# Kernel optimization log

Measured on AMD Instinct MI355X. Metric: run time of the kernel, lower is better.

The kernel has to match this reference:

```python
import jax, jax.numpy as jnp
import numpy as np

B, S, T = 1024, 1024, 32  # batch, seq_len, num_tags


def setup_inputs() -> dict:
    key = jax.random.key(0)
    k1, k2, k3, k4 = jax.random.split(key, 4)
    logits = jax.random.normal(k1, (B, S, T), dtype=jnp.float32)
    transitions = jax.random.normal(k2, (T, T), dtype=jnp.float32)
    tags = jax.random.randint(k3, (B, S), 0, T)
    lengths = jax.random.randint(k4, (B,), 1, S + 1)
    return {"logits": logits, "transitions": transitions, "tags": tags, "lengths": lengths}


def _forward_alg(logits, transitions):
    # viterbi_0 = logits[:, 0, :]; then for t>=1:
    # v_next[b, j] = logsumexp_i(v[b, i] + trans[i, j]) + logits[b, t, j]
    v0 = logits[:, 0, :]  # (B, T)
    emits = jnp.swapaxes(logits[:, 1:, :], 0, 1)  # (S-1, B, T)

    def step(v, emit_t):
        v_next = jax.nn.logsumexp(v[:, :, None] + transitions[None, :, :], axis=1) + emit_t
        return v_next, None

    v_final, _ = jax.lax.scan(step, v0, emits)
    return jax.nn.logsumexp(v_final, axis=1)  # (B,)


def _score_sentence(logits, transitions, tags, lengths):
    # emission scores of gold tags, masked to t < length (note: original ignores
    # lengths in the forward algorithm but uses them here, faithfully reproduced)
    emit = jnp.take_along_axis(logits, tags[:, :, None], axis=2)[..., 0]  # (B, S)
    pos = jnp.arange(S)
    emit_mask = (pos[None, :] < lengths[:, None]).astype(logits.dtype)
    score = jnp.sum(emit * emit_mask, axis=1)
    # transition scores trans[tags[t-1], tags[t]] for 1 <= t < length
    trans_sc = transitions[tags[:, :-1], tags[:, 1:]]  # (B, S-1)
    trans_mask = (pos[None, 1:] < lengths[:, None]).astype(logits.dtype)
    score = score + jnp.sum(trans_sc * trans_mask, axis=1)
    return score  # (B,)


def reference(logits, transitions, tags, lengths):
    log_z = _forward_alg(logits, transitions)
    gold = _score_sentence(logits, transitions, tags, lengths)
    return jnp.mean(log_z - gold)
```

## Files before the change

kernel.cpp:

```cpp
#include <hip/hip_runtime.h>

#define NB 1024
#define NS 1024
#define NT 32
#define L2E 1.44269504088896340736f
#define LN2 0.69314718055994530942f

typedef short        bfrag  __attribute__((ext_vector_type(8)));
typedef float        cfrag  __attribute__((ext_vector_type(16)));
typedef __bf16       bf16x2 __attribute__((ext_vector_type(2)));
typedef float        f32x8  __attribute__((ext_vector_type(8)));
typedef float        f32x4  __attribute__((ext_vector_type(4)));
typedef float        f32x2  __attribute__((ext_vector_type(2)));
typedef unsigned int u32;
typedef unsigned int u32x4  __attribute__((ext_vector_type(4)));

__device__ __forceinline__ float fexp2(float x){ return __builtin_amdgcn_exp2f(x); }
__device__ __forceinline__ float flog2(float x){ return __builtin_amdgcn_logf(x); }

__device__ __forceinline__ u32 pkbf_rne(float a, float b){
    f32x2 t; t.x = a; t.y = b;
    return __builtin_bit_cast(u32, __builtin_convertvector(t, bf16x2));
}
__device__ __forceinline__ u32 pkbf_t(float a, float b){
    return __builtin_amdgcn_perm(__builtin_bit_cast(u32, b),
                                 __builtin_bit_cast(u32, a), 0x07060302u);
}
__device__ __forceinline__ bfrag mk_afrag(f32x8 v){
    u32x4 r;
    r[0] = pkbf_rne(v[0], v[1]); r[1] = pkbf_rne(v[2], v[3]);
    r[2] = pkbf_rne(v[4], v[5]); r[3] = pkbf_rne(v[6], v[7]);
    return __builtin_bit_cast(bfrag, r);
}

__device__ __forceinline__ int rho(int k){
    int bb = (k >> 2) & 3;
    return (bb == 1 || bb == 2) ? (k ^ 12) : k;
}

template<int N> struct ic { static constexpr int value = N; };
union accu { cfrag c; f32x2 p[8]; };
union q4u  { f32x4 v; f32x2 p[2]; };

__global__ __launch_bounds__(256, 8) void crf_chunk(
    const float* __restrict__ logits, const float* __restrict__ trans,
    const int* __restrict__ tags, const int* __restrict__ lens,
    u32* __restrict__ wmat, float* __restrict__ woff, float* __restrict__ gpart)
{
    __shared__ __align__(16) float dscall[4 * 512];

    const int tid = threadIdx.x;
    const int wv  = tid >> 6, lt = tid & 63;
    const int m   = lt & 31,  h  = lt >> 5;
    const int bc  = blockIdx.x * 4 + wv;
    const int b   = bc >> 3,  c  = bc & 7;
    float* dsc = dscall + wv * 512;

    const float* base = logits + (size_t)b * NS * NT;
    const int    len  = lens[b];
    const int    tb   = b * NS;

    f32x8 Et0, Et1;
    #pragma unroll
    for (int j = 0; j < 8; j++){
        Et0[j] = fexp2(L2E * trans[rho(     8*h + j)*NT + m]);
        Et1[j] = fexp2(L2E * trans[rho(16 + 8*h + j)*NT + m]);
    }
    const bfrag A0f = mk_afrag(Et0);
    const bfrag A1f = mk_afrag(Et1);

    u32x4 B0v, B1v;
    #pragma unroll
    for (int d = 0; d < 4; d++){
        int k0 = 8*h + 2*d;      u32 v = 0;
        if (rho(k0)     == m) v |= 0x3F80u;
        if (rho(k0 + 1) == m) v |= 0x3F800000u;
        B0v[d] = v;
        int k1 = 16 + 8*h + 2*d; v = 0;
        if (rho(k1)     == m) v |= 0x3F80u;
        if (rho(k1 + 1) == m) v |= 0x3F800000u;
        B1v[d] = v;
    }

    cfrag zacc;
    #pragma unroll
    for (int q = 0; q < 16; q++) zacc[q] = 0.0f;

    int   offi = 0;
    float exf  = 0.0f;
    float g    = 0.0f;
    const int tbeg = c*128 + 1;

    float eA[4], eB[4];

    auto issue = [&](float (&e)[4], int k){
        const int t0 = tbeg + k*8 + 4*h;
        #pragma unroll
        for (int i = 0; i < 4; i++){
            int t = t0 + i; t = t > (NS-1) ? (NS-1) : t;
            e[i] = base[t*NT + m];
        }
    };
    auto commit = [&](float (&e)[4], int k){
        float* sp = dsc + (k & 1)*256 + (4*h)*32 + m;
        float a0 = (h == 0) ? -exf : 0.0f;
        sp[0]    = fexp2(fmaf(L2E, e[0], a0));
        sp[32]   = fexp2(L2E * e[1]);
        sp[64]   = fexp2(L2E * e[2]);
        sp[96]   = fexp2(L2E * e[3]);
        const int t0 = tbeg + k*8 + 4*h;
        int tp = tags[tb + t0 - 1];
        #pragma unroll
        for (int i = 0; i < 4; i++){
            int t  = t0 + i;
            int tc = tags[tb + (t > (NS-1) ? (NS-1) : t)];
            float contrib = e[i] + trans[tp*NT + tc];
            if (t < len && m == tc) g += contrib;
            tp = tc;
        }
    };

    auto exref = [&](float ref)->int{
        u32 xb = __builtin_bit_cast(u32, ref);
        u32 xf = __builtin_amdgcn_readfirstlane(xb);
        int ex = (int)((xf >> 23) & 0xFFu) - 127;
        return ex < -120 ? -120 : (ex > 120 ? 120 : ex);
    };

    auto procN = [&](int k, bool defer, auto nstc){
        constexpr int NST = decltype(nstc)::value;
        const float* db = dsc + (k & 1)*256 + 4*h;
        #pragma unroll
        for (int i = 0; i < NST; i++){
            accu acc;
            acc.c = __builtin_amdgcn_mfma_f32_32x32x16_bf16(
                        A0f, __builtin_bit_cast(bfrag, B0v), zacc, 0, 0, 0);
            acc.c = __builtin_amdgcn_mfma_f32_32x32x16_bf16(
                        A1f, __builtin_bit_cast(bfrag, B1v), acc.c, 0, 0, 0);

            q4u d0, d1, d2, d3;
            d0.v = *(const f32x4*)(db + i*32 +  0);
            d1.v = *(const f32x4*)(db + i*32 +  8);
            d2.v = *(const f32x4*)(db + i*32 + 16);
            d3.v = *(const f32x4*)(db + i*32 + 24);
            acc.p[0] *= d0.p[0]; acc.p[1] *= d0.p[1];
            acc.p[2] *= d1.p[0]; acc.p[3] *= d1.p[1];
            acc.p[4] *= d2.p[0]; acc.p[5] *= d2.p[1];
            acc.p[6] *= d3.p[0]; acc.p[7] *= d3.p[1];

            if (i == 3){
                int ex = exref(fmaxf(acc.c[0], acc.c[8]));
                offi += ex;
                f32x2 s2;
                s2.x = s2.y = __builtin_bit_cast(float, (u32)(127 - ex) << 23);
                #pragma unroll
                for (int q = 0; q < 8; q++) acc.p[q] *= s2;
            }
            if (i == 7 && defer){
                int ex = exref(fmaxf(acc.c[0], acc.c[8]));
                offi += ex;
                exf = (float)ex;
            }

            B0v[0] = pkbf_t(acc.c[0],  acc.c[1]);  B0v[1] = pkbf_t(acc.c[2],  acc.c[3]);
            B0v[2] = pkbf_t(acc.c[4],  acc.c[5]);  B0v[3] = pkbf_t(acc.c[6],  acc.c[7]);
            B1v[0] = pkbf_t(acc.c[8],  acc.c[9]);  B1v[1] = pkbf_t(acc.c[10], acc.c[11]);
            B1v[2] = pkbf_t(acc.c[12], acc.c[13]); B1v[3] = pkbf_t(acc.c[14], acc.c[15]);
        }
    };

    issue(eA, 0); commit(eA, 0);
    #pragma unroll 1
    for (int k = 0; k < 14; k += 2){
        issue(eB, k + 1);
        procN(k, true, ic<8>{});
        commit(eB, k + 1);
        issue(eA, k + 2);
        procN(k + 1, true, ic<8>{});
        commit(eA, k + 2);
    }
    issue(eB, 15);
    procN(14, true, ic<8>{});
    commit(eB, 15);
    if (c != 7) procN(15, false, ic<8>{});
    else        procN(15, false, ic<7>{});

    const size_t mb = (size_t)bc * 512;
    #pragma unroll
    for (int d = 0; d < 4; d++){
        wmat[mb + d*64 + lt]     = B0v[d];
        wmat[mb + (4+d)*64 + lt] = B1v[d];
    }
    if (lt == 0) woff[bc] = (float)offi;

    #pragma unroll
    for (int d = 1; d < 64; d <<= 1) g += __shfl_xor(g, d, 64);
    if (lt == 0) gpart[bc] = g;
}

__global__ __launch_bounds__(64) void crf_combine(
    const float* __restrict__ logits, const int* __restrict__ tags,
    const u32* __restrict__ wmat, const float* __restrict__ woff,
    const float* __restrict__ gpart, float* __restrict__ out)
{
    __shared__ __align__(16) float ldsU[NT];

    const int tid = threadIdx.x;
    const int m   = tid & 31;
    const int b   = blockIdx.x;
    const float* lgb = logits + (size_t)b * NS * NT;

    const int   tg0 = tags[(size_t)b * NS];
    const float e0  = lgb[tg0];

    float4 gp0 = ((const float4*)(gpart + b*8))[0];
    float4 gp1 = ((const float4*)(gpart + b*8))[1];
    const float gsum = (gp0.x + gp0.y) + (gp0.z + gp0.w)
                     + (gp1.x + gp1.y) + (gp1.z + gp1.w);

    float offs[8];
    #pragma unroll
    for (int cc = 0; cc < 8; cc++) offs[cc] = woff[b*8 + cc];

    float v    = fexp2(L2E * lgb[m]);
    float voff = 0.0f;

    const int n  = m;
    const int bb = (n >> 2) & 3;
    const int nn = (bb == 1 || bb == 2) ? (n ^ 12) : n;
    const int f  = nn >> 4;
    const int hh = (nn >> 3) & 1;
    const int di = f*4 + ((nn >> 1) & 3);
    const int lo = nn & 1;

    auto ldrow = [&](int cc, uint4 (&md)[8]){
        const uint4* mp = (const uint4*)(wmat + (size_t)(b*8 + cc)*512 + di*64 + hh*32);
        #pragma unroll
        for (int qq = 0; qq < 8; qq++) md[qq] = mp[qq];
    };

    uint4 mdA[8], mdB[8];
    ldrow(0, mdA);

    #pragma unroll
    for (int cc = 0; cc < 8; cc++){
        uint4 (&cur)[8] = (cc & 1) ? mdB : mdA;
        uint4 (&nxt)[8] = (cc & 1) ? mdA : mdB;
        if (cc < 7) ldrow(cc + 1, nxt);

        float w  = flog2(v) + offs[cc];
        float mw = w;
        #pragma unroll
        for (int d = 1; d <= 16; d <<= 1) mw = fmaxf(mw, __shfl_xor(mw, d, 64));
        float u = fexp2(w - mw);
        if (tid < 32) ldsU[m] = u;
        __syncthreads();

        float acc = 0.0f;
        #pragma unroll
        for (int qq = 0; qq < 8; qq++){
            uint4  md = cur[qq];
            float4 uu = ((const float4*)ldsU)[qq];
            float v0 = __builtin_bit_cast(float, lo ? (md.x & 0xFFFF0000u) : (md.x << 16));
            float v1 = __builtin_bit_cast(float, lo ? (md.y & 0xFFFF0000u) : (md.y << 16));
            float v2 = __builtin_bit_cast(float, lo ? (md.z & 0xFFFF0000u) : (md.z << 16));
            float v3 = __builtin_bit_cast(float, lo ? (md.w & 0xFFFF0000u) : (md.w << 16));
            acc = fmaf(v0, uu.x, acc);
            acc = fmaf(v1, uu.y, acc);
            acc = fmaf(v2, uu.z, acc);
            acc = fmaf(v3, uu.w, acc);
        }
        v = acc;
        voff += mw;
        __syncthreads();
    }

    float s = v;
    #pragma unroll
    for (int d = 1; d <= 16; d <<= 1) s += __shfl_xor(s, d, 64);
    if (tid == 0){
        float logz = LN2 * (voff + flog2(s));
        atomicAdd(out, (logz - gsum - e0) * (1.0f / (float)NB));
    }
}

extern "C" void kernel_launch(void* const* d_in, const int* in_sizes, int n_in,
                              void* d_out, int out_size, void* d_ws, size_t ws_size,
                              hipStream_t stream) {
    const float* logits = (const float*)d_in[0];
    const float* trans  = (const float*)d_in[1];
    const int*   tags   = (const int*)d_in[2];
    const int*   lens   = (const int*)d_in[3];

    u32*   wmat  = (u32*)d_ws;
    float* woff  = (float*)(wmat + 8192*512);
    float* gpart = woff + 8192;

    hipMemsetAsync(d_out, 0, sizeof(float), stream);
    crf_chunk  <<<2048, 256, 0, stream>>>(logits, trans, tags, lens, wmat, woff, gpart);
    crf_combine<<<1024,  64, 0, stream>>>(logits, tags, wmat, woff, gpart, (float*)d_out);
}
```

Before: 309.0 us.

## Move gold-path scoring from chunk kernel into combine kernel and drop memset

The gold-score gather (tags, transitions, emissions) is removed from the latency-critical chunk kernel's commit loop and recomputed in the combine kernel, which now runs 256 threads per batch and stages tags and transitions in LDS. The output zeroing moves from a separate memset into the first thread of the chunk kernel, removing one launch. This shortens the serial recurrence critical path at the cost of extra gathered loads in the combine kernel. The zeroing relies on the chunk kernel finishing before the combine kernel's atomics, which stream ordering provides.

```diff
diff --git a/kernel.cpp b/kernel.cpp
--- a/kernel.cpp
+++ b/kernel.cpp
@@ -44,8 +44,7 @@
 
 __global__ __launch_bounds__(256, 8) void crf_chunk(
     const float* __restrict__ logits, const float* __restrict__ trans,
-    const int* __restrict__ tags, const int* __restrict__ lens,
-    u32* __restrict__ wmat, float* __restrict__ woff, float* __restrict__ gpart)
+    u32* __restrict__ wmat, float* __restrict__ woff, float* __restrict__ outz)
 {
     __shared__ __align__(16) float dscall[4 * 512];
 
@@ -56,9 +55,9 @@
     const int b   = bc >> 3,  c  = bc & 7;
     float* dsc = dscall + wv * 512;
 
+    if (blockIdx.x == 0 && tid == 0) *outz = 0.0f;
+
     const float* base = logits + (size_t)b * NS * NT;
-    const int    len  = lens[b];
-    const int    tb   = b * NS;
 
     f32x8 Et0, Et1;
     #pragma unroll
@@ -88,7 +87,6 @@
 
     int   offi = 0;
     float exf  = 0.0f;
-    float g    = 0.0f;
     const int tbeg = c*128 + 1;
 
     float eA[4], eB[4];
@@ -108,16 +106,6 @@
         sp[32]   = fexp2(L2E * e[1]);
         sp[64]   = fexp2(L2E * e[2]);
         sp[96]   = fexp2(L2E * e[3]);
-        const int t0 = tbeg + k*8 + 4*h;
-        int tp = tags[tb + t0 - 1];
-        #pragma unroll
-        for (int i = 0; i < 4; i++){
-            int t  = t0 + i;
-            int tc = tags[tb + (t > (NS-1) ? (NS-1) : t)];
-            float contrib = e[i] + trans[tp*NT + tc];
-            if (t < len && m == tc) g += contrib;
-            tp = tc;
-        }
     };
 
     auto exref = [&](float ref)->int{
@@ -192,31 +180,49 @@
         wmat[mb + (4+d)*64 + lt] = B1v[d];
     }
     if (lt == 0) woff[bc] = (float)offi;
-
-    #pragma unroll
-    for (int d = 1; d < 64; d <<= 1) g += __shfl_xor(g, d, 64);
-    if (lt == 0) gpart[bc] = g;
-}
-
-__global__ __launch_bounds__(64) void crf_combine(
-    const float* __restrict__ logits, const int* __restrict__ tags,
+}
+
+__global__ __launch_bounds__(256) void crf_combine(
+    const float* __restrict__ logits, const float* __restrict__ trans,
+    const int* __restrict__ tags, const int* __restrict__ lens,
     const u32* __restrict__ wmat, const float* __restrict__ woff,
-    const float* __restrict__ gpart, float* __restrict__ out)
+    float* __restrict__ out)
 {
+    __shared__ __align__(16) float ldsT[NT*NT];
+    __shared__ __align__(16) int   ldsTag[NS];
     __shared__ __align__(16) float ldsU[NT];
+    __shared__ float red[4];
 
     const int tid = threadIdx.x;
     const int m   = tid & 31;
     const int b   = blockIdx.x;
+    const int len = lens[b];
     const float* lgb = logits + (size_t)b * NS * NT;
 
-    const int   tg0 = tags[(size_t)b * NS];
-    const float e0  = lgb[tg0];
-
-    float4 gp0 = ((const float4*)(gpart + b*8))[0];
-    float4 gp1 = ((const float4*)(gpart + b*8))[1];
-    const float gsum = (gp0.x + gp0.y) + (gp0.z + gp0.w)
-                     + (gp1.x + gp1.y) + (gp1.z + gp1.w);
+    ((float4*)ldsT)[tid] = ((const float4*)trans)[tid];
+    ((int4*)ldsTag)[tid] = ((const int4*)(tags + (size_t)b * NS))[tid];
+    __syncthreads();
+
+    const int t0 = tid * 4;
+    int4 tgv = ((const int4*)ldsTag)[tid];
+    int  prv = ldsTag[tid == 0 ? 0 : t0 - 1];
+    int tgs[5] = {prv, tgv.x, tgv.y, tgv.z, tgv.w};
+
+    float g = 0.0f;
+    #pragma unroll
+    for (int i = 0; i < 4; i++){
+        int t = t0 + i;
+        if (t < len){
+            float e  = lgb[t*NT + tgs[i+1]];
+            float tr = (t >= 1) ? ldsT[tgs[i]*NT + tgs[i+1]] : 0.0f;
+            g += e + tr;
+        }
+    }
+    #pragma unroll
+    for (int d = 1; d < 64; d <<= 1) g += __shfl_xor(g, d, 64);
+    if ((tid & 63) == 0) red[tid >> 6] = g;
+    __syncthreads();
+    const float gsum = red[0] + red[1] + red[2] + red[3];
 
     float offs[8];
     #pragma unroll
@@ -280,7 +286,7 @@
     for (int d = 1; d <= 16; d <<= 1) s += __shfl_xor(s, d, 64);
     if (tid == 0){
         float logz = LN2 * (voff + flog2(s));
-        atomicAdd(out, (logz - gsum - e0) * (1.0f / (float)NB));
+        atomicAdd(out, (logz - gsum) * (1.0f / (float)NB));
     }
 }
 
@@ -292,11 +298,10 @@
     const int*   tags   = (const int*)d_in[2];
     const int*   lens   = (const int*)d_in[3];
 
-    u32*   wmat  = (u32*)d_ws;
-    float* woff  = (float*)(wmat + 8192*512);
-    float* gpart = woff + 8192;
-
-    hipMemsetAsync(d_out, 0, sizeof(float), stream);
-    crf_chunk  <<<2048, 256, 0, stream>>>(logits, trans, tags, lens, wmat, woff, gpart);
-    crf_combine<<<1024,  64, 0, stream>>>(logits, tags, wmat, woff, gpart, (float*)d_out);
-}
+    u32*   wmat = (u32*)d_ws;
+    float* woff = (float*)(wmat + 8192*512);
+
+    crf_chunk  <<<2048, 256, 0, stream>>>(logits, trans, wmat, woff, (float*)d_out);
+    crf_combine<<<1024, 256, 0, stream>>>(logits, trans, tags, lens, wmat, woff,
+                                          (float*)d_out);
+}
```

New measurement: 261.7 us. 15.3% less time.

## Fuse chunk and combine kernels via last-block-done atomic counter

Applied to the files above, without the earlier changes.

Merges the per-chunk forward kernel and the per-batch combine kernel into one launch. The last wave to finish a batch row, detected through an atomic counter, runs the 8-step matrix combine. The combine now broadcasts the vector with wave shuffles instead of LDS and barriers, and rescales by a power-of-two exponent instead of log/exp. The gold-path score is moved out of the inner commit loop into a single vectorized pass per wave that accumulates atomically. This removes a kernel launch and the intermediate gpart round trip, at the cost of extra atomics and threadfences and a serialized tail on the last-arriving waves.

```diff
diff --git a/kernel.cpp b/kernel.cpp
--- a/kernel.cpp
+++ b/kernel.cpp
@@ -32,6 +32,9 @@
     r[2] = pkbf_rne(v[4], v[5]); r[3] = pkbf_rne(v[6], v[7]);
     return __builtin_bit_cast(bfrag, r);
 }
+__device__ __forceinline__ float ubf(u32 x, int lo){
+    return __builtin_bit_cast(float, lo ? (x & 0xFFFF0000u) : (x << 16));
+}
 
 __device__ __forceinline__ int rho(int k){
     int bb = (k >> 2) & 3;
@@ -42,10 +45,13 @@
 union accu { cfrag c; f32x2 p[8]; };
 union q4u  { f32x4 v; f32x2 p[2]; };
 
-__global__ __launch_bounds__(256, 8) void crf_chunk(
+__global__ __launch_bounds__(256, 8) void crf_fused(
     const float* __restrict__ logits, const float* __restrict__ trans,
     const int* __restrict__ tags, const int* __restrict__ lens,
-    u32* __restrict__ wmat, float* __restrict__ woff, float* __restrict__ gpart)
+    u32* __restrict__ wmat, float* __restrict__ woff,
+    float* __restrict__ gacc, int* __restrict__ cnt,
+    float* __restrict__ outac, int* __restrict__ nfin,
+    float* __restrict__ out)
 {
     __shared__ __align__(16) float dscall[4 * 512];
 
@@ -88,7 +94,6 @@
 
     int   offi = 0;
     float exf  = 0.0f;
-    float g    = 0.0f;
     const int tbeg = c*128 + 1;
 
     float eA[4], eB[4];
@@ -108,16 +113,6 @@
         sp[32]   = fexp2(L2E * e[1]);
         sp[64]   = fexp2(L2E * e[2]);
         sp[96]   = fexp2(L2E * e[3]);
-        const int t0 = tbeg + k*8 + 4*h;
-        int tp = tags[tb + t0 - 1];
-        #pragma unroll
-        for (int i = 0; i < 4; i++){
-            int t  = t0 + i;
-            int tc = tags[tb + (t > (NS-1) ? (NS-1) : t)];
-            float contrib = e[i] + trans[tp*NT + tc];
-            if (t < len && m == tc) g += contrib;
-            tp = tc;
-        }
     };
 
     auto exref = [&](float ref)->int{
@@ -193,94 +188,87 @@
     }
     if (lt == 0) woff[bc] = (float)offi;
 
-    #pragma unroll
-    for (int d = 1; d < 64; d <<= 1) g += __shfl_xor(g, d, 64);
-    if (lt == 0) gpart[bc] = g;
-}
-
-__global__ __launch_bounds__(64) void crf_combine(
-    const float* __restrict__ logits, const int* __restrict__ tags,
-    const u32* __restrict__ wmat, const float* __restrict__ woff,
-    const float* __restrict__ gpart, float* __restrict__ out)
-{
-    __shared__ __align__(16) float ldsU[NT];
-
-    const int tid = threadIdx.x;
-    const int m   = tid & 31;
-    const int b   = blockIdx.x;
-    const float* lgb = logits + (size_t)b * NS * NT;
-
-    const int   tg0 = tags[(size_t)b * NS];
-    const float e0  = lgb[tg0];
-
-    float4 gp0 = ((const float4*)(gpart + b*8))[0];
-    float4 gp1 = ((const float4*)(gpart + b*8))[1];
-    const float gsum = (gp0.x + gp0.y) + (gp0.z + gp0.w)
-                     + (gp1.x + gp1.y) + (gp1.z + gp1.w);
+    {
+        const int t1 = tbeg + 2*lt;
+        const int t2 = t1 + 1;
+        const int i2 = t2 > (NS-1) ? (NS-1) : t2;
+        const int g0 = tags[tb + t1 - 1];
+        const int g1 = tags[tb + t1];
+        const int g2 = tags[tb + i2];
+        float gg = 0.0f;
+        if (t1 < len) gg += base[t1*NT + g1] + trans[g0*NT + g1];
+        if (t2 < len) gg += base[t2*NT + g2] + trans[g1*NT + g2];
+        #pragma unroll
+        for (int d = 1; d < 64; d <<= 1) gg += __shfl_xor(gg, d, 64);
+        if (lt == 0){
+            if (c == 0) gg += base[tags[tb]];
+            atomicAdd(&gacc[b], gg);
+        }
+    }
+
+    __threadfence();
+    int old = 0;
+    if (lt == 0) old = atomicAdd(&cnt[b], 1);
+    old = __shfl(old, 0, 64);
+    if (old != 7) return;
+
+    __threadfence();
+
+    const int n   = lt & 31;
+    const int bb2 = (n >> 2) & 3;
+    const int nn  = (bb2 == 1 || bb2 == 2) ? (n ^ 12) : n;
+    const int segbase = (nn >> 4)*256 + ((nn >> 3) & 1)*32 + ((nn >> 1) & 3)*64;
+    const int lo  = nn & 1;
+    const u32* wbm = wmat + (size_t)b * 8 * 512 + segbase;
 
     float offs[8];
     #pragma unroll
     for (int cc = 0; cc < 8; cc++) offs[cc] = woff[b*8 + cc];
 
-    float v    = fexp2(L2E * lgb[m]);
+    float v    = fexp2(L2E * base[n]);
     float voff = 0.0f;
 
-    const int n  = m;
-    const int bb = (n >> 2) & 3;
-    const int nn = (bb == 1 || bb == 2) ? (n ^ 12) : n;
-    const int f  = nn >> 4;
-    const int hh = (nn >> 3) & 1;
-    const int di = f*4 + ((nn >> 1) & 3);
-    const int lo = nn & 1;
-
-    auto ldrow = [&](int cc, uint4 (&md)[8]){
-        const uint4* mp = (const uint4*)(wmat + (size_t)(b*8 + cc)*512 + di*64 + hh*32);
+    #pragma unroll
+    for (int cc = 0; cc < 8; cc++){
+        uint4 md[8];
+        const uint4* mp = (const uint4*)(wbm + cc*512);
         #pragma unroll
         for (int qq = 0; qq < 8; qq++) md[qq] = mp[qq];
-    };
-
-    uint4 mdA[8], mdB[8];
-    ldrow(0, mdA);
-
-    #pragma unroll
-    for (int cc = 0; cc < 8; cc++){
-        uint4 (&cur)[8] = (cc & 1) ? mdB : mdA;
-        uint4 (&nxt)[8] = (cc & 1) ? mdA : mdB;
-        if (cc < 7) ldrow(cc + 1, nxt);
-
-        float w  = flog2(v) + offs[cc];
-        float mw = w;
-        #pragma unroll
-        for (int d = 1; d <= 16; d <<= 1) mw = fmaxf(mw, __shfl_xor(mw, d, 64));
-        float u = fexp2(w - mw);
-        if (tid < 32) ldsU[m] = u;
-        __syncthreads();
 
         float acc = 0.0f;
         #pragma unroll
         for (int qq = 0; qq < 8; qq++){
-            uint4  md = cur[qq];
-            float4 uu = ((const float4*)ldsU)[qq];
-            float v0 = __builtin_bit_cast(float, lo ? (md.x & 0xFFFF0000u) : (md.x << 16));
-            float v1 = __builtin_bit_cast(float, lo ? (md.y & 0xFFFF0000u) : (md.y << 16));
-            float v2 = __builtin_bit_cast(float, lo ? (md.z & 0xFFFF0000u) : (md.z << 16));
-            float v3 = __builtin_bit_cast(float, lo ? (md.w & 0xFFFF0000u) : (md.w << 16));
-            acc = fmaf(v0, uu.x, acc);
-            acc = fmaf(v1, uu.y, acc);
-            acc = fmaf(v2, uu.z, acc);
-            acc = fmaf(v3, uu.w, acc);
-        }
-        v = acc;
-        voff += mw;
-        __syncthreads();
+            float u0 = __shfl(v, 4*qq + 0, 64);
+            float u1 = __shfl(v, 4*qq + 1, 64);
+            float u2 = __shfl(v, 4*qq + 2, 64);
+            float u3 = __shfl(v, 4*qq + 3, 64);
+            acc = fmaf(ubf(md[qq].x, lo), u0, acc);
+            acc = fmaf(ubf(md[qq].y, lo), u1, acc);
+            acc = fmaf(ubf(md[qq].z, lo), u2, acc);
+            acc = fmaf(ubf(md[qq].w, lo), u3, acc);
+        }
+        float mx = acc;
+        #pragma unroll
+        for (int d = 1; d <= 16; d <<= 1) mx = fmaxf(mx, __shfl_xor(mx, d, 64));
+        int ex = exref(mx);
+        v = acc * __builtin_bit_cast(float, (u32)(127 - ex) << 23);
+        voff += (float)ex + offs[cc];
     }
 
     float s = v;
     #pragma unroll
     for (int d = 1; d <= 16; d <<= 1) s += __shfl_xor(s, d, 64);
-    if (tid == 0){
+
+    if (lt == 0){
+        float gold = atomicAdd(&gacc[b], 0.0f);
         float logz = LN2 * (voff + flog2(s));
-        atomicAdd(out, (logz - gsum - e0) * (1.0f / (float)NB));
+        atomicAdd(outac, (logz - gold) * (1.0f / (float)NB));
+        __threadfence();
+        int t2e = atomicAdd(nfin, 1);
+        if (t2e == NB - 1){
+            __threadfence();
+            *out = atomicAdd(outac, 0.0f);
+        }
     }
 }
 
@@ -293,10 +281,15 @@
     const int*   lens   = (const int*)d_in[3];
 
     u32*   wmat  = (u32*)d_ws;
-    float* woff  = (float*)(wmat + 8192*512);
-    float* gpart = woff + 8192;
-
-    hipMemsetAsync(d_out, 0, sizeof(float), stream);
-    crf_chunk  <<<2048, 256, 0, stream>>>(logits, trans, tags, lens, wmat, woff, gpart);
-    crf_combine<<<1024,  64, 0, stream>>>(logits, tags, wmat, woff, gpart, (float*)d_out);
-}
+    float* woff  = (float*)((char*)d_ws + 16u*1024u*1024u);
+    char*  ctl   = (char*)d_ws + 16u*1024u*1024u + 32u*1024u;
+    float* gacc  = (float*)ctl;
+    int*   cnt   = (int*)(ctl + 4096);
+    float* outac = (float*)(ctl + 8192);
+    int*   nfin  = (int*)(ctl + 8192 + 4);
+
+    hipMemsetAsync(ctl, 0, 8448, stream);
+    crf_fused<<<2048, 256, 0, stream>>>(logits, trans, tags, lens,
+                                        wmat, woff, gacc, cnt, outac, nfin,
+                                        (float*)d_out);
+}
```

After: 944.8 us. 206% more time.
